# Performance work log

Hardware: AMD Instinct MI355X
Metric: run time of the kernel (lower is better)

The kernel has to match this reference:

```python
import jax, jax.numpy as jnp
import numpy as np

NUM_USERS = 50000
NUM_ITEMS = 100000
EMB_DIM = 64
N_LAYERS = 3
N_EDGES = 1200000
N_NODES = NUM_USERS + NUM_ITEMS


def setup_inputs() -> dict:
    key = jax.random.key(0)
    k1, k2, k3, k4, k5 = jax.random.split(key, 5)
    user_emb = jax.random.normal(k1, (NUM_USERS, EMB_DIM), dtype=jnp.float32)
    item_emb = jax.random.normal(k2, (NUM_ITEMS, EMB_DIM), dtype=jnp.float32)
    adj_rows = jax.random.randint(k3, (N_EDGES,), 0, N_NODES, dtype=jnp.int32)
    adj_cols = jax.random.randint(k4, (N_EDGES,), 0, N_NODES, dtype=jnp.int32)
    adj_vals = jax.random.uniform(k5, (N_EDGES,), dtype=jnp.float32)
    return {"user_emb": user_emb, "item_emb": item_emb,
            "adj_rows": adj_rows, "adj_cols": adj_cols, "adj_vals": adj_vals}


def reference(user_emb, item_emb, adj_rows, adj_cols, adj_vals):
    num_users = user_emb.shape[0]
    n_nodes = num_users + item_emb.shape[0]

    def spmm(x):
        # y[r] += v * x[c] for each nnz (r, c, v)  -- COO SpMM
        msgs = adj_vals[:, None] * x[adj_cols]          # [E, D]
        return jax.ops.segment_sum(msgs, adj_rows, num_segments=n_nodes)

    all_emb = jnp.concatenate([user_emb, item_emb], axis=0)  # [N, D]
    # fused multi-hop propagation: accumulate layer outputs instead of stacking
    acc = all_emb
    for _ in range(N_LAYERS):
        all_emb = spmm(all_emb)
        acc = acc + all_emb
    final_embs = acc / jnp.float32(N_LAYERS + 1)  # mean over (n_layers+1) hops
    users = final_embs[:num_users]
    items = final_embs[num_users:]
    return (users, items)
```

## Files before the change

### kernel.cpp

```cpp
#include <hip/hip_runtime.h>

#define EMB 64
#define BKT_BITS 9
#define BKT_ROWS (1 << BKT_BITS)
#define BKT_CAP 4608
#define MAX_BKT 512
#define CO_EDGES 4096

typedef float f32x4 __attribute__((ext_vector_type(4)));

__global__ __launch_bounds__(256) void scatter_coarse(
        const int* __restrict__ rows,
        const int* __restrict__ cols,
        const float* __restrict__ vals,
        int* __restrict__ bcur,
        int2* __restrict__ es, int n_edges, int nbkt) {
    __shared__ int lcnt[MAX_BKT];
    __shared__ int lbase[MAX_BKT];
    int tid = threadIdx.x;
    for (int i = tid; i < nbkt; i += 256) lcnt[i] = 0;
    __syncthreads();
    int e0 = blockIdx.x * CO_EDGES;
    int e1 = min(e0 + CO_EDGES, n_edges);
    for (int e = e0 + tid; e < e1; e += 256)
        atomicAdd(&lcnt[rows[e] >> BKT_BITS], 1);
    __syncthreads();
    for (int i = tid; i < nbkt; i += 256) {
        int c = lcnt[i];
        lbase[i] = c ? atomicAdd(&bcur[i], c) : 0;
    }
    __syncthreads();
    for (int e = e0 + tid; e < e1; e += 256) {
        int r = rows[e];
        int b = r >> BKT_BITS;
        int p = atomicAdd(&lbase[b], 1);
        if (p < BKT_CAP)
            es[(size_t)b * BKT_CAP + p] =
                make_int2(cols[e] | ((r & (BKT_ROWS - 1)) << 18),
                          __float_as_int(vals[e]));
    }
}

__global__ __launch_bounds__(512) void scatter_fine(
        const int* __restrict__ bcur,
        int2* __restrict__ es,
        int2* __restrict__ rbe, int n_nodes, int nbkt) {
    __shared__ int2 stage[BKT_CAP];
    __shared__ int rcnt[BKT_ROWS];
    __shared__ int rsc[BKT_ROWS];
    int b = blockIdx.x;
    int tid = threadIdx.x;
    int cnt = min(bcur[b], BKT_CAP);
    int base = b * BKT_CAP;
    rcnt[tid] = 0;
    __syncthreads();
    for (int j = tid; j < cnt; j += BKT_ROWS) {
        int2 e = es[base + j];
        stage[j] = e;
        atomicAdd(&rcnt[e.x >> 18], 1);
    }
    __syncthreads();
    int v = rcnt[tid];
    rsc[tid] = v;
    __syncthreads();
    for (int d = 1; d < BKT_ROWS; d <<= 1) {
        int t = (tid >= d) ? rsc[tid - d] : 0;
        __syncthreads();
        rsc[tid] += t;
        __syncthreads();
    }
    int excl = rsc[tid] - v;
    rcnt[tid] = excl;
    int r = (b << BKT_BITS) + tid;
    if (r < n_nodes) rbe[r] = make_int2(base + excl, base + excl + v);
    __syncthreads();
    for (int j = tid; j < cnt; j += BKT_ROWS) {
        int2 e = stage[j];
        int p = atomicAdd(&rcnt[e.x >> 18], 1);
        es[base + p] = make_int2(e.x & 0x3FFFF, e.y);
    }
}

__device__ __forceinline__ const float4* xrow(const float* xu,
                                              const float* xi,
                                              int nu, int col) {
    return (const float4*)((col < nu) ? (xu + (size_t)col * EMB)
                                      : (xi + (size_t)(col - nu) * EMB));
}

__global__ __launch_bounds__(256) void spmm_csr(
        const int2* __restrict__ rbe,
        const int2* __restrict__ es,
        const float* __restrict__ xu,
        const float* __restrict__ xi,
        int nu,
        float4* __restrict__ y,
        const float4* __restrict__ y1,
        const float4* __restrict__ y2,
        const float* __restrict__ x0u,
        const float* __restrict__ x0i,
        int n_nodes, int mode) {
    int gid = blockIdx.x * blockDim.x + threadIdx.x;
    int r = gid >> 4;
    if (r >= n_nodes) return;
    int q = gid & 15;
    int2 be = rbe[r];
    int beg = be.x;
    int end = be.y;
    float4 a = make_float4(0.f, 0.f, 0.f, 0.f);
    int j = beg;
    for (; j + 4 <= end; j += 4) {
        int2 e0 = es[j];
        int2 e1 = es[j + 1];
        int2 e2 = es[j + 2];
        int2 e3 = es[j + 3];
        float4 x0 = xrow(xu, xi, nu, e0.x)[q];
        float4 x1 = xrow(xu, xi, nu, e1.x)[q];
        float4 x2 = xrow(xu, xi, nu, e2.x)[q];
        float4 x3 = xrow(xu, xi, nu, e3.x)[q];
        float v0 = __int_as_float(e0.y);
        float v1 = __int_as_float(e1.y);
        float v2 = __int_as_float(e2.y);
        float v3 = __int_as_float(e3.y);
        a.x += v0 * x0.x; a.y += v0 * x0.y; a.z += v0 * x0.z; a.w += v0 * x0.w;
        a.x += v1 * x1.x; a.y += v1 * x1.y; a.z += v1 * x1.z; a.w += v1 * x1.w;
        a.x += v2 * x2.x; a.y += v2 * x2.y; a.z += v2 * x2.z; a.w += v2 * x2.w;
        a.x += v3 * x3.x; a.y += v3 * x3.y; a.z += v3 * x3.z; a.w += v3 * x3.w;
    }
    if (j + 2 <= end) {
        int2 e0 = es[j];
        int2 e1 = es[j + 1];
        float4 x0 = xrow(xu, xi, nu, e0.x)[q];
        float4 x1 = xrow(xu, xi, nu, e1.x)[q];
        float v0 = __int_as_float(e0.y);
        float v1 = __int_as_float(e1.y);
        a.x += v0 * x0.x; a.y += v0 * x0.y; a.z += v0 * x0.z; a.w += v0 * x0.w;
        a.x += v1 * x1.x; a.y += v1 * x1.y; a.z += v1 * x1.z; a.w += v1 * x1.w;
        j += 2;
    }
    if (j < end) {
        int2 e0 = es[j];
        float4 x0 = xrow(xu, xi, nu, e0.x)[q];
        float v0 = __int_as_float(e0.y);
        a.x += v0 * x0.x; a.y += v0 * x0.y; a.z += v0 * x0.z; a.w += v0 * x0.w;
    }
    size_t o = (size_t)r * (EMB / 4) + q;
    if (mode < 2) {
        __builtin_nontemporal_store(*(const f32x4*)&a, (f32x4*)&y[o]);
    } else {
        const float4* b0 = (r < nu)
            ? ((const float4*)x0u + (size_t)r * (EMB / 4))
            : ((const float4*)x0i + (size_t)(r - nu) * (EMB / 4));
        float4 f0 = b0[q];
        float4 a1 = y1[o];
        float4 a2 = y2[o];
        float4 ac;
        ac.x = 0.25f * (f0.x + a1.x + a2.x + a.x);
        ac.y = 0.25f * (f0.y + a1.y + a2.y + a.y);
        ac.z = 0.25f * (f0.z + a1.z + a2.z + a.z);
        ac.w = 0.25f * (f0.w + a1.w + a2.w + a.w);
        __builtin_nontemporal_store(*(const f32x4*)&ac, (f32x4*)&y[o]);
    }
}

extern "C" void kernel_launch(void* const* d_in, const int* in_sizes, int n_in,
                              void* d_out, int out_size, void* d_ws, size_t ws_size,
                              hipStream_t stream) {
    const float* ue   = (const float*)d_in[0];
    const float* ie   = (const float*)d_in[1];
    const int*   rows = (const int*)d_in[2];
    const int*   cols = (const int*)d_in[3];
    const float* vals = (const float*)d_in[4];
    float* out = (float*)d_out;

    const int num_users = in_sizes[0] / EMB;
    const int num_items = in_sizes[1] / EMB;
    const int n_nodes   = num_users + num_items;
    const int n_edges   = in_sizes[2];

    const int nbkt = (n_nodes + BKT_ROWS - 1) >> BKT_BITS;

    const size_t buf_elems = (size_t)n_nodes * EMB;
    float* y2buf = (float*)d_ws;
    int2*  es    = (int2*)(y2buf + buf_elems);
    int2*  rbe   = es + (size_t)nbkt * BKT_CAP;
    int*   bcur  = (int*)(rbe + n_nodes);

    hipMemsetAsync(bcur, 0, (size_t)nbkt * sizeof(int), stream);

    {
        int cblocks = (n_edges + CO_EDGES - 1) / CO_EDGES;
        scatter_coarse<<<cblocks, 256, 0, stream>>>(rows, cols, vals,
                                                    bcur, es, n_edges, nbkt);
        scatter_fine<<<nbkt, BKT_ROWS, 0, stream>>>(bcur, es, rbe,
                                                    n_nodes, nbkt);
    }

    {
        int threads = 256;
        int blocks  = (n_nodes * 16 + threads - 1) / threads;
        spmm_csr<<<blocks, threads, 0, stream>>>(
            rbe, es, ue, ie, num_users,
            (float4*)out, nullptr, nullptr, nullptr, nullptr, n_nodes, 0);
        spmm_csr<<<blocks, threads, 0, stream>>>(
            rbe, es, (const float*)out, (const float*)out + (size_t)num_users * EMB,
            num_users,
            (float4*)y2buf, nullptr, nullptr, nullptr, nullptr, n_nodes, 1);
        spmm_csr<<<blocks, threads, 0, stream>>>(
            rbe, es, y2buf, y2buf + (size_t)num_users * EMB, num_users,
            (float4*)out, (const float4*)out, (const float4*)y2buf,
            ue, ie, n_nodes, 2);
    }
}
```

Baseline: 291.8 us.

## Fuse bucket scatter and three SpMM passes into one cooperative persistent kernel

Replaces the memset and the five separate launches (coarse scatter, fine scatter, three SpMM layers) with a single cooperative kernel that uses grid-wide syncs between phases. Work inside each phase is spread with grid-stride loops, the coarse chunk size drops from 4096 to 2048 edges, and blocks grow to 512 threads. Layer-1/2 stores change from nontemporal to normal stores so the next layer may find its input in cache. The aim is to remove launch gaps and tail effects between dependent kernels. The cost is fewer resident threads and grid.sync overhead, with the old multi-kernel path kept as a fallback.

```diff
diff --git a/kernel.cpp b/kernel.cpp
--- a/kernel.cpp
+++ b/kernel.cpp
@@ -1,85 +1,17 @@
 #include <hip/hip_runtime.h>
+#include <hip/hip_cooperative_groups.h>
+
+namespace cg = cooperative_groups;
 
 #define EMB 64
 #define BKT_BITS 9
 #define BKT_ROWS (1 << BKT_BITS)
 #define BKT_CAP 4608
 #define MAX_BKT 512
-#define CO_EDGES 4096
+#define CO_EDGES 2048
 
 typedef float f32x4 __attribute__((ext_vector_type(4)));
 
-__global__ __launch_bounds__(256) void scatter_coarse(
-        const int* __restrict__ rows,
-        const int* __restrict__ cols,
-        const float* __restrict__ vals,
-        int* __restrict__ bcur,
-        int2* __restrict__ es, int n_edges, int nbkt) {
-    __shared__ int lcnt[MAX_BKT];
-    __shared__ int lbase[MAX_BKT];
-    int tid = threadIdx.x;
-    for (int i = tid; i < nbkt; i += 256) lcnt[i] = 0;
-    __syncthreads();
-    int e0 = blockIdx.x * CO_EDGES;
-    int e1 = min(e0 + CO_EDGES, n_edges);
-    for (int e = e0 + tid; e < e1; e += 256)
-        atomicAdd(&lcnt[rows[e] >> BKT_BITS], 1);
-    __syncthreads();
-    for (int i = tid; i < nbkt; i += 256) {
-        int c = lcnt[i];
-        lbase[i] = c ? atomicAdd(&bcur[i], c) : 0;
-    }
-    __syncthreads();
-    for (int e = e0 + tid; e < e1; e += 256) {
-        int r = rows[e];
-        int b = r >> BKT_BITS;
-        int p = atomicAdd(&lbase[b], 1);
-        if (p < BKT_CAP)
-            es[(size_t)b * BKT_CAP + p] =
-                make_int2(cols[e] | ((r & (BKT_ROWS - 1)) << 18),
-                          __float_as_int(vals[e]));
-    }
-}
-
-__global__ __launch_bounds__(512) void scatter_fine(
-        const int* __restrict__ bcur,
-        int2* __restrict__ es,
-        int2* __restrict__ rbe, int n_nodes, int nbkt) {
-    __shared__ int2 stage[BKT_CAP];
-    __shared__ int rcnt[BKT_ROWS];
-    __shared__ int rsc[BKT_ROWS];
-    int b = blockIdx.x;
-    int tid = threadIdx.x;
-    int cnt = min(bcur[b], BKT_CAP);
-    int base = b * BKT_CAP;
-    rcnt[tid] = 0;
-    __syncthreads();
-    for (int j = tid; j < cnt; j += BKT_ROWS) {
-        int2 e = es[base + j];
-        stage[j] = e;
-        atomicAdd(&rcnt[e.x >> 18], 1);
-    }
-    __syncthreads();
-    int v = rcnt[tid];
-    rsc[tid] = v;
-    __syncthreads();
-    for (int d = 1; d < BKT_ROWS; d <<= 1) {
-        int t = (tid >= d) ? rsc[tid - d] : 0;
-        __syncthreads();
-        rsc[tid] += t;
-        __syncthreads();
-    }
-    int excl = rsc[tid] - v;
-    rcnt[tid] = excl;
-    int r = (b << BKT_BITS) + tid;
-    if (r < n_nodes) rbe[r] = make_int2(base + excl, base + excl + v);
-    __syncthreads();
-    for (int j = tid; j < cnt; j += BKT_ROWS) {
-        int2 e = stage[j];
-        int p = atomicAdd(&rcnt[e.x >> 18], 1);
-        es[base + p] = make_int2(e.x & 0x3FFFF, e.y);
-    }
-}
 
 __device__ __forceinline__ const float4* xrow(const float* xu,
                                               const float* xi,
@@ -88,79 +20,219 @@
                                       : (xi + (size_t)(col - nu) * EMB));
 }
 
-__global__ __launch_bounds__(256) void spmm_csr(
-        const int2* __restrict__ rbe,
-        const int2* __restrict__ es,
-        const float* __restrict__ xu,
-        const float* __restrict__ xi,
-        int nu,
-        float4* __restrict__ y,
-        const float4* __restrict__ y1,
-        const float4* __restrict__ y2,
-        const float* __restrict__ x0u,
-        const float* __restrict__ x0i,
+__device__ void coarse_body(const int* __restrict__ rows,
+                            const int* __restrict__ cols,
+                            const float* __restrict__ vals,
+                            int* bcur, int2* __restrict__ es,
+                            int n_edges, int nbkt,
+                            int* lcnt, int* lbase,
+                            int cstart, int cstride) {
+    int tid = threadIdx.x;
+    int nchunk = (n_edges + CO_EDGES - 1) / CO_EDGES;
+    for (int c = cstart; c < nchunk; c += cstride) {
+        for (int i = tid; i < nbkt; i += 512) lcnt[i] = 0;
+        __syncthreads();
+        int e0 = c * CO_EDGES;
+        int e1 = min(e0 + CO_EDGES, n_edges);
+        for (int e = e0 + tid; e < e1; e += 512)
+            atomicAdd(&lcnt[rows[e] >> BKT_BITS], 1);
+        __syncthreads();
+        for (int i = tid; i < nbkt; i += 512) {
+            int cc = lcnt[i];
+            lbase[i] = cc ? atomicAdd(&bcur[i], cc) : 0;
+        }
+        __syncthreads();
+        for (int e = e0 + tid; e < e1; e += 512) {
+            int r = rows[e];
+            int b = r >> BKT_BITS;
+            int p = atomicAdd(&lbase[b], 1);
+            if (p < BKT_CAP)
+                es[(size_t)b * BKT_CAP + p] =
+                    make_int2(cols[e] | ((r & (BKT_ROWS - 1)) << 18),
+                              __float_as_int(vals[e]));
+        }
+        __syncthreads();
+    }
+}
+
+__device__ void fine_body(const int* bcur, int2* __restrict__ es,
+                          int2* __restrict__ rbe, int n_nodes, int nbkt,
+                          int2* stage, int* rcnt, int* rsc,
+                          int bstart, int bstride) {
+    int tid = threadIdx.x;
+    for (int b = bstart; b < nbkt; b += bstride) {
+        int cnt = min(bcur[b], BKT_CAP);
+        int base = b * BKT_CAP;
+        rcnt[tid] = 0;
+        __syncthreads();
+        for (int j = tid; j < cnt; j += BKT_ROWS) {
+            int2 e = es[base + j];
+            stage[j] = e;
+            atomicAdd(&rcnt[e.x >> 18], 1);
+        }
+        __syncthreads();
+        int v = rcnt[tid];
+        rsc[tid] = v;
+        __syncthreads();
+        for (int d = 1; d < BKT_ROWS; d <<= 1) {
+            int t = (tid >= d) ? rsc[tid - d] : 0;
+            __syncthreads();
+            rsc[tid] += t;
+            __syncthreads();
+        }
+        int excl = rsc[tid] - v;
+        rcnt[tid] = excl;
+        int r = (b << BKT_BITS) + tid;
+        if (r < n_nodes) rbe[r] = make_int2(base + excl, base + excl + v);
+        __syncthreads();
+        for (int j = tid; j < cnt; j += BKT_ROWS) {
+            int2 e = stage[j];
+            int p = atomicAdd(&rcnt[e.x >> 18], 1);
+            es[base + p] = make_int2(e.x & 0x3FFFF, e.y);
+        }
+        __syncthreads();
+    }
+}
+
+__device__ void spmm_body(const int2* __restrict__ rbe,
+                          const int2* __restrict__ es,
+                          const float* xu, const float* xi, int nu,
+                          float4* y, const float4* y1, const float4* y2,
+                          const float* __restrict__ x0u,
+                          const float* __restrict__ x0i,
+                          int n_nodes, int mode, int gid0, int gstride) {
+    int lanes = n_nodes * 16;
+    for (int gid = gid0; gid < lanes; gid += gstride) {
+        int r = gid >> 4;
+        int q = gid & 15;
+        int2 be = rbe[r];
+        int beg = be.x;
+        int end = be.y;
+        float4 a = make_float4(0.f, 0.f, 0.f, 0.f);
+        int j = beg;
+        for (; j + 4 <= end; j += 4) {
+            int2 e0 = es[j];
+            int2 e1 = es[j + 1];
+            int2 e2 = es[j + 2];
+            int2 e3 = es[j + 3];
+            float4 x0 = xrow(xu, xi, nu, e0.x)[q];
+            float4 x1 = xrow(xu, xi, nu, e1.x)[q];
+            float4 x2 = xrow(xu, xi, nu, e2.x)[q];
+            float4 x3 = xrow(xu, xi, nu, e3.x)[q];
+            float v0 = __int_as_float(e0.y);
+            float v1 = __int_as_float(e1.y);
+            float v2 = __int_as_float(e2.y);
+            float v3 = __int_as_float(e3.y);
+            a.x += v0 * x0.x; a.y += v0 * x0.y; a.z += v0 * x0.z; a.w += v0 * x0.w;
+            a.x += v1 * x1.x; a.y += v1 * x1.y; a.z += v1 * x1.z; a.w += v1 * x1.w;
+            a.x += v2 * x2.x; a.y += v2 * x2.y; a.z += v2 * x2.z; a.w += v2 * x2.w;
+            a.x += v3 * x3.x; a.y += v3 * x3.y; a.z += v3 * x3.z; a.w += v3 * x3.w;
+        }
+        if (j + 2 <= end) {
+            int2 e0 = es[j];
+            int2 e1 = es[j + 1];
+            float4 x0 = xrow(xu, xi, nu, e0.x)[q];
+            float4 x1 = xrow(xu, xi, nu, e1.x)[q];
+            float v0 = __int_as_float(e0.y);
+            float v1 = __int_as_float(e1.y);
+            a.x += v0 * x0.x; a.y += v0 * x0.y; a.z += v0 * x0.z; a.w += v0 * x0.w;
+            a.x += v1 * x1.x; a.y += v1 * x1.y; a.z += v1 * x1.z; a.w += v1 * x1.w;
+            j += 2;
+        }
+        if (j < end) {
+            int2 e0 = es[j];
+            float4 x0 = xrow(xu, xi, nu, e0.x)[q];
+            float v0 = __int_as_float(e0.y);
+            a.x += v0 * x0.x; a.y += v0 * x0.y; a.z += v0 * x0.z; a.w += v0 * x0.w;
+        }
+        size_t o = (size_t)r * (EMB / 4) + q;
+        if (mode < 2) {
+            y[o] = a;
+        } else {
+            const float4* b0 = (r < nu)
+                ? ((const float4*)x0u + (size_t)r * (EMB / 4))
+                : ((const float4*)x0i + (size_t)(r - nu) * (EMB / 4));
+            float4 f0 = b0[q];
+            float4 a1 = y1[o];
+            float4 a2 = y2[o];
+            float4 ac;
+            ac.x = 0.25f * (f0.x + a1.x + a2.x + a.x);
+            ac.y = 0.25f * (f0.y + a1.y + a2.y + a.y);
+            ac.z = 0.25f * (f0.z + a1.z + a2.z + a.z);
+            ac.w = 0.25f * (f0.w + a1.w + a2.w + a.w);
+            __builtin_nontemporal_store(*(const f32x4*)&ac, (f32x4*)&y[o]);
+        }
+    }
+}
+
+__global__ __launch_bounds__(512, 6) void mega(
+        const int* __restrict__ rows, const int* __restrict__ cols,
+        const float* __restrict__ vals,
+        int* bcur, int2* __restrict__ es, int2* __restrict__ rbe,
+        const float* __restrict__ ue, const float* __restrict__ ie,
+        float* y2buf, float* out,
+        int nu, int n_nodes, int n_edges, int nbkt) {
+    cg::grid_group grid = cg::this_grid();
+    __shared__ int2 stage[BKT_CAP];
+    __shared__ int rcnt[BKT_ROWS];
+    __shared__ int rsc[BKT_ROWS];
+    int gid0 = blockIdx.x * blockDim.x + threadIdx.x;
+    int gstride = gridDim.x * blockDim.x;
+
+    for (int i = gid0; i < nbkt; i += gstride) bcur[i] = 0;
+    grid.sync();
+
+    coarse_body(rows, cols, vals, bcur, es, n_edges, nbkt,
+                (int*)stage, (int*)stage + MAX_BKT, blockIdx.x, gridDim.x);
+    grid.sync();
+
+    fine_body(bcur, es, rbe, n_nodes, nbkt, stage, rcnt, rsc,
+              blockIdx.x, gridDim.x);
+    grid.sync();
+
+    spmm_body(rbe, es, ue, ie, nu, (float4*)out,
+              nullptr, nullptr, nullptr, nullptr, n_nodes, 0, gid0, gstride);
+    grid.sync();
+
+    spmm_body(rbe, es, out, out + (size_t)nu * EMB, nu, (float4*)y2buf,
+              nullptr, nullptr, nullptr, nullptr, n_nodes, 1, gid0, gstride);
+    grid.sync();
+
+    spmm_body(rbe, es, y2buf, y2buf + (size_t)nu * EMB, nu, (float4*)out,
+              (const float4*)out, (const float4*)y2buf, ue, ie,
+              n_nodes, 2, gid0, gstride);
+}
+
+
+__global__ __launch_bounds__(512) void k_coarse(
+        const int* __restrict__ rows, const int* __restrict__ cols,
+        const float* __restrict__ vals, int* bcur, int2* __restrict__ es,
+        int n_edges, int nbkt) {
+    __shared__ int lcnt[MAX_BKT];
+    __shared__ int lbase[MAX_BKT];
+    coarse_body(rows, cols, vals, bcur, es, n_edges, nbkt,
+                lcnt, lbase, blockIdx.x, gridDim.x);
+}
+
+__global__ __launch_bounds__(512) void k_fine(
+        const int* bcur, int2* __restrict__ es, int2* __restrict__ rbe,
+        int n_nodes, int nbkt) {
+    __shared__ int2 stage[BKT_CAP];
+    __shared__ int rcnt[BKT_ROWS];
+    __shared__ int rsc[BKT_ROWS];
+    fine_body(bcur, es, rbe, n_nodes, nbkt, stage, rcnt, rsc,
+              blockIdx.x, gridDim.x);
+}
+
+__global__ __launch_bounds__(512) void k_spmm(
+        const int2* __restrict__ rbe, const int2* __restrict__ es,
+        const float* xu, const float* xi, int nu,
+        float4* y, const float4* y1, const float4* y2,
+        const float* __restrict__ x0u, const float* __restrict__ x0i,
         int n_nodes, int mode) {
-    int gid = blockIdx.x * blockDim.x + threadIdx.x;
-    int r = gid >> 4;
-    if (r >= n_nodes) return;
-    int q = gid & 15;
-    int2 be = rbe[r];
-    int beg = be.x;
-    int end = be.y;
-    float4 a = make_float4(0.f, 0.f, 0.f, 0.f);
-    int j = beg;
-    for (; j + 4 <= end; j += 4) {
-        int2 e0 = es[j];
-        int2 e1 = es[j + 1];
-        int2 e2 = es[j + 2];
-        int2 e3 = es[j + 3];
-        float4 x0 = xrow(xu, xi, nu, e0.x)[q];
-        float4 x1 = xrow(xu, xi, nu, e1.x)[q];
-        float4 x2 = xrow(xu, xi, nu, e2.x)[q];
-        float4 x3 = xrow(xu, xi, nu, e3.x)[q];
-        float v0 = __int_as_float(e0.y);
-        float v1 = __int_as_float(e1.y);
-        float v2 = __int_as_float(e2.y);
-        float v3 = __int_as_float(e3.y);
-        a.x += v0 * x0.x; a.y += v0 * x0.y; a.z += v0 * x0.z; a.w += v0 * x0.w;
-        a.x += v1 * x1.x; a.y += v1 * x1.y; a.z += v1 * x1.z; a.w += v1 * x1.w;
-        a.x += v2 * x2.x; a.y += v2 * x2.y; a.z += v2 * x2.z; a.w += v2 * x2.w;
-        a.x += v3 * x3.x; a.y += v3 * x3.y; a.z += v3 * x3.z; a.w += v3 * x3.w;
-    }
-    if (j + 2 <= end) {
-        int2 e0 = es[j];
-        int2 e1 = es[j + 1];
-        float4 x0 = xrow(xu, xi, nu, e0.x)[q];
-        float4 x1 = xrow(xu, xi, nu, e1.x)[q];
-        float v0 = __int_as_float(e0.y);
-        float v1 = __int_as_float(e1.y);
-        a.x += v0 * x0.x; a.y += v0 * x0.y; a.z += v0 * x0.z; a.w += v0 * x0.w;
-        a.x += v1 * x1.x; a.y += v1 * x1.y; a.z += v1 * x1.z; a.w += v1 * x1.w;
-        j += 2;
-    }
-    if (j < end) {
-        int2 e0 = es[j];
-        float4 x0 = xrow(xu, xi, nu, e0.x)[q];
-        float v0 = __int_as_float(e0.y);
-        a.x += v0 * x0.x; a.y += v0 * x0.y; a.z += v0 * x0.z; a.w += v0 * x0.w;
-    }
-    size_t o = (size_t)r * (EMB / 4) + q;
-    if (mode < 2) {
-        __builtin_nontemporal_store(*(const f32x4*)&a, (f32x4*)&y[o]);
-    } else {
-        const float4* b0 = (r < nu)
-            ? ((const float4*)x0u + (size_t)r * (EMB / 4))
-            : ((const float4*)x0i + (size_t)(r - nu) * (EMB / 4));
-        float4 f0 = b0[q];
-        float4 a1 = y1[o];
-        float4 a2 = y2[o];
-        float4 ac;
-        ac.x = 0.25f * (f0.x + a1.x + a2.x + a.x);
-        ac.y = 0.25f * (f0.y + a1.y + a2.y + a.y);
-        ac.z = 0.25f * (f0.z + a1.z + a2.z + a.z);
-        ac.w = 0.25f * (f0.w + a1.w + a2.w + a.w);
-        __builtin_nontemporal_store(*(const f32x4*)&ac, (f32x4*)&y[o]);
-    }
+    spmm_body(rbe, es, xu, xi, nu, y, y1, y2, x0u, x0i, n_nodes, mode,
+              blockIdx.x * blockDim.x + threadIdx.x,
+              gridDim.x * blockDim.x);
 }
 
 extern "C" void kernel_launch(void* const* d_in, const int* in_sizes, int n_in,
@@ -177,8 +249,7 @@
     const int num_items = in_sizes[1] / EMB;
     const int n_nodes   = num_users + num_items;
     const int n_edges   = in_sizes[2];
-
-    const int nbkt = (n_nodes + BKT_ROWS - 1) >> BKT_BITS;
+    const int nbkt      = (n_nodes + BKT_ROWS - 1) >> BKT_BITS;
 
     const size_t buf_elems = (size_t)n_nodes * EMB;
     float* y2buf = (float*)d_ws;
@@ -186,27 +257,42 @@
     int2*  rbe   = es + (size_t)nbkt * BKT_CAP;
     int*   bcur  = (int*)(rbe + n_nodes);
 
-    hipMemsetAsync(bcur, 0, (size_t)nbkt * sizeof(int), stream);
-
-    {
-        int cblocks = (n_edges + CO_EDGES - 1) / CO_EDGES;
-        scatter_coarse<<<cblocks, 256, 0, stream>>>(rows, cols, vals,
-                                                    bcur, es, n_edges, nbkt);
-        scatter_fine<<<nbkt, BKT_ROWS, 0, stream>>>(bcur, es, rbe,
-                                                    n_nodes, nbkt);
-    }
-
-    {
-        int threads = 256;
-        int blocks  = (n_nodes * 16 + threads - 1) / threads;
-        spmm_csr<<<blocks, threads, 0, stream>>>(
-            rbe, es, ue, ie, num_users,
-            (float4*)out, nullptr, nullptr, nullptr, nullptr, n_nodes, 0);
-        spmm_csr<<<blocks, threads, 0, stream>>>(
-            rbe, es, (const float*)out, (const float*)out + (size_t)num_users * EMB,
-            num_users,
+    static int grid_blocks = 0;
+    if (grid_blocks == 0) {
+        int occ = 0, cus = 0, dev = 0;
+        hipGetDevice(&dev);
+        hipOccupancyMaxActiveBlocksPerMultiprocessor(&occ, mega, 512, 0);
+        hipDeviceGetAttribute(&cus, hipDeviceAttributeMultiprocessorCount, dev);
+        if (occ < 1) occ = 1;
+        if (occ > 4) occ = 4;
+        if (cus < 1) cus = 256;
+        grid_blocks = occ * cus;
+    }
+
+    int nu = num_users, nn = n_nodes, ne = n_edges, nb = nbkt;
+    void* args[] = { (void*)&rows, (void*)&cols, (void*)&vals,
+                     (void*)&bcur, (void*)&es, (void*)&rbe,
+                     (void*)&ue, (void*)&ie, (void*)&y2buf, (void*)&out,
+                     (void*)&nu, (void*)&nn, (void*)&ne, (void*)&nb };
+    hipError_t err = hipLaunchCooperativeKernel(
+        mega, dim3(grid_blocks), dim3(512), args, 0, stream);
+
+    if (err != hipSuccess) {
+        (void)hipGetLastError();
+        hipMemsetAsync(bcur, 0, (size_t)nbkt * sizeof(int), stream);
+        int nchunk = (n_edges + CO_EDGES - 1) / CO_EDGES;
+        k_coarse<<<nchunk, 512, 0, stream>>>(rows, cols, vals, bcur, es,
+                                             n_edges, nbkt);
+        k_fine<<<nbkt, 512, 0, stream>>>(bcur, es, rbe, n_nodes, nbkt);
+        int blocks = (n_nodes * 16 + 511) / 512;
+        k_spmm<<<blocks, 512, 0, stream>>>(
+            rbe, es, ue, ie, num_users, (float4*)out,
+            nullptr, nullptr, nullptr, nullptr, n_nodes, 0);
+        k_spmm<<<blocks, 512, 0, stream>>>(
+            rbe, es, (const float*)out,
+            (const float*)out + (size_t)num_users * EMB, num_users,
             (float4*)y2buf, nullptr, nullptr, nullptr, nullptr, n_nodes, 1);
-        spmm_csr<<<blocks, threads, 0, stream>>>(
+        k_spmm<<<blocks, 512, 0, stream>>>(
             rbe, es, y2buf, y2buf + (size_t)num_users * EMB, num_users,
             (float4*)out, (const float4*)out, (const float4*)y2buf,
             ue, ie, n_nodes, 2);
```

Result: slower. 597.5 us (+104.7%).
